# Performance work log

Measured on AMD Instinct MI355X. Metric: run time of the kernel, lower is better.

Reference implementation:

```python
import jax, jax.numpy as jnp
import numpy as np

B, S, D = 2, 512, 256      # batch, seq_len, d_model
N = 16                     # d_state
DC = 4                     # d_conv
DI = 2 * D                 # d_inner
CHUNK = 32                 # scan remat chunk size (S % CHUNK == 0)


def setup_inputs() -> dict:
    key = jax.random.key(0)
    ks = jax.random.split(key, 10)
    sc = 0.02
    return {
        "x": jax.random.normal(ks[0], (B, S, D), jnp.float32),
        "adjacency_matrix": jax.random.uniform(ks[1], (B, S, S), dtype=jnp.float32),
        "ln_w": jnp.ones((D,), jnp.float32),
        "ln_b": jnp.zeros((D,), jnp.float32),
        "W_in": jax.random.normal(ks[2], (2 * DI, D), jnp.float32) * sc,
        "conv_w": jax.random.normal(ks[3], (DI, DI, DC), jnp.float32) * sc,
        "conv_b": jnp.zeros((DI,), jnp.float32),
        "W_xp": jax.random.normal(ks[4], (2 * N + 1, DI), jnp.float32) * sc,
        "W_dt": jax.random.normal(ks[5], (DI, 1), jnp.float32) * sc,
        "b_dt": jnp.zeros((DI,), jnp.float32),
        "Wr": jax.random.normal(ks[6], (N, N), jnp.float32) * sc,
        "br": jnp.zeros((N,), jnp.float32),
        "W_out": jax.random.normal(ks[7], (D, DI), jnp.float32) * sc,
    }


def _forward(x, adj, ln_w, ln_b, W_in, conv_w, conv_b, W_xp, W_dt, b_dt, Wr, br, W_out):
    residual = x
    # LayerNorm (biased variance, eps=1e-5, matching nn.LayerNorm)
    mu = x.mean(-1, keepdims=True)
    var = ((x - mu) ** 2).mean(-1, keepdims=True)
    xn = (x - mu) * jax.lax.rsqrt(var + 1e-5) * ln_w + ln_b
    # in_proj (no bias), chunk into x branch and gate z
    xz = xn @ W_in.T                                  # [B,S,2*DI]
    xp, z = xz[..., :DI], xz[..., DI:]
    # causal-ish conv1d with padding d_conv-1, then slice to seq_len
    xc = jax.lax.conv_general_dilated(
        xp.transpose(0, 2, 1), conv_w, (1,), [(DC - 1, DC - 1)],
        dimension_numbers=("NCH", "OIH", "NCH"))
    xc = (xc + conv_b[None, :, None])[..., :S].transpose(0, 2, 1)  # [B,S,DI]
    x_act = jax.nn.silu(xc)
    # x_proj (no bias) -> delta(1), B(N), C(N)
    ssm = x_act @ W_xp.T                              # [B,S,2N+1]
    delta = jax.nn.softplus(ssm[..., :1] @ W_dt.T + b_dt)  # [B,S,DI]
    Bm, Cm = ssm[..., 1:1 + N], ssm[..., 1 + N:]      # [B,S,N]
    pos = jnp.arange(S)

    def step(carry, xs):
        h, hist = xs_carry = carry
        t, d_t, B_t, C_t, x_t, a_t = xs
        # exponential-decay state update: h [B,DI,N]
        h = h * jnp.exp(-d_t)[..., None] + x_t[..., None] * B_t[:, None, :]
        # adjacency-gated, degree-normalized aggregation over prior states
        w = a_t * (pos < t)                           # [B,S], zeros for s>=t
        deg = jnp.maximum(w.sum(-1), 1.0)             # clamp(min=1.0)
        g = jnp.einsum('bs,sbdn->bdn', w, hist) / deg[:, None, None]
        boost = 0.1 * jax.nn.silu(g @ Wr.T + br)
        # torch skips the boost when t==0 or all causal weights are zero
        h = h + jnp.where((t > 0) & jnp.any(w > 0), boost, jnp.zeros_like(boost))
        hist = hist.at[t].set(h)
        y = jnp.einsum('bdn,bn->bd', h, C_t)
        return (h, hist), y

    xs = (pos,
          delta.transpose(1, 0, 2), Bm.transpose(1, 0, 2), Cm.transpose(1, 0, 2),
          x_act.transpose(1, 0, 2), adj.transpose(1, 0, 2))
    nchunks = S // CHUNK
    xs = jax.tree_util.tree_map(lambda a: a.reshape(nchunks, CHUNK, *a.shape[1:]), xs)
    carry0 = (jnp.zeros((B, DI, N), jnp.float32),
              jnp.zeros((S, B, DI, N), jnp.float32))

    @jax.checkpoint
    def chunk_body(carry, xs_c):
        return jax.lax.scan(step, carry, xs_c)

    _, ys = jax.lax.scan(chunk_body, carry0, xs)
    y = ys.reshape(S, B, DI).transpose(1, 0, 2)       # [B,S,DI]
    return (y * jax.nn.silu(z)) @ W_out.T + residual


def reference(x, adjacency_matrix, ln_w, ln_b, W_in, conv_w, conv_b, W_xp, W_dt, b_dt, Wr, br, W_out):
    return _forward(x, adjacency_matrix, ln_w, ln_b, W_in, conv_w, conv_b,
                    W_xp, W_dt, b_dt, Wr, br, W_out)
```

## Files before the change

### kernel.cpp

```cpp
#include <hip/hip_runtime.h>
#include <math.h>

static constexpr int B  = 2;
static constexpr int S  = 512;
static constexpr int D  = 256;
static constexpr int N  = 16;
static constexpr int DI = 512;
static constexpr int CHUNK = 32;
static constexpr int NCHUNK = S / CHUNK;
static constexpr int NL = NCHUNK / 2;
static constexpr int DN = DI * N;
static constexpr int NSLOT = 8;

typedef unsigned int uint32;
typedef unsigned short ushort16;
using bf16x8 = __attribute__((ext_vector_type(8))) short;
using f32x4  = __attribute__((ext_vector_type(4))) float;

__device__ __forceinline__ ushort16 f2bf(float f) {
    uint32 u = __float_as_uint(f);
    u = (u + 0x7fffu + ((u >> 16) & 1u)) >> 16;
    return (ushort16)u;
}
__device__ __forceinline__ float bflo(uint32 u) { return __uint_as_float(u << 16); }
__device__ __forceinline__ float bfhi(uint32 u) { return __uint_as_float(u & 0xffff0000u); }
__device__ __forceinline__ float bf2f(ushort16 u) { return __uint_as_float(((uint32)u) << 16); }
__device__ __forceinline__ uint32 pk2(float a, float b) {
    return (uint32)(ushort16)f2bf(a) | ((uint32)(ushort16)f2bf(b) << 16);
}
template<int K>
__device__ __forceinline__ float rork(float x) {
    return __uint_as_float((uint32)__builtin_amdgcn_mov_dpp(
        (int)__float_as_uint(x), 0x120 + K, 0xf, 0xf, false));
}
__device__ __forceinline__ size_t htIdx(int b, int dn, int sb) {
    return ((size_t)(b * (S / 32) + sb) * DN + dn) * 32;
}

__global__ void ln_k(const float* __restrict__ x, const float* __restrict__ w,
                     const float* __restrict__ bias, ushort16* __restrict__ xnb) {
    int row = blockIdx.x;
    int lane = threadIdx.x;
    float4 v = *(const float4*)(x + row * D + lane * 4);
    float s = v.x + v.y + v.z + v.w;
    float q = v.x * v.x + v.y * v.y + v.z * v.z + v.w * v.w;
    for (int m = 1; m < 64; m <<= 1) { s += __shfl_xor(s, m); q += __shfl_xor(q, m); }
    float mu  = s * (1.0f / D);
    float var = q * (1.0f / D) - mu * mu;
    float rs  = rsqrtf(var + 1e-5f);
    float4 wv = *(const float4*)(w + lane * 4);
    float4 bv = *(const float4*)(bias + lane * 4);
    float4 o;
    o.x = (v.x - mu) * rs * wv.x + bv.x;
    o.y = (v.y - mu) * rs * wv.y + bv.y;
    o.z = (v.z - mu) * rs * wv.z + bv.z;
    o.w = (v.w - mu) * rs * wv.w + bv.w;
    uint2 pk;
    pk.x = pk2(o.x, o.y);
    pk.y = pk2(o.z, o.w);
    *(uint2*)(xnb + row * D + lane * 4) = pk;
}

template<int MODE>
__global__ __launch_bounds__(256) void gemmb_k(const ushort16* __restrict__ A,
                                               const float* __restrict__ W,
                                               const float* __restrict__ res,
                                               float* __restrict__ C,
                                               ushort16* __restrict__ xpb,
                                               float* __restrict__ zs,
                                               int M, int Nc, int K) {
    __shared__ __align__(16) short As[64 * 40];
    __shared__ __align__(16) short Ws[64 * 40];
    int tid = threadIdx.x;
    int l = tid & 63, wid = tid >> 6;
    int wm = wid & 1, wn = wid >> 1;
    int row0 = blockIdx.y * 64, col0 = blockIdx.x * 64;
    int r = tid >> 2, kseg = (tid & 3) * 8;
    f32x4 acc[2][2] = {};
    for (int k0 = 0; k0 < K; k0 += 32) {
        *(uint4*)&As[r * 40 + kseg] = *(const uint4*)(A + (size_t)(row0 + r) * K + k0 + kseg);
        {
            const float* wrow = W + (size_t)(col0 + r) * K + k0 + kseg;
            float4 w0 = *(const float4*)wrow;
            float4 w1 = *(const float4*)(wrow + 4);
            uint4 q;
            q.x = pk2(w0.x, w0.y); q.y = pk2(w0.z, w0.w);
            q.z = pk2(w1.x, w1.y); q.w = pk2(w1.z, w1.w);
            *(uint4*)&Ws[r * 40 + kseg] = q;
        }
        __syncthreads();
        bf16x8 aF[2], bF[2];
        #pragma unroll
        for (int am = 0; am < 2; ++am)
            aF[am] = *(const bf16x8*)&As[(wm * 32 + am * 16 + (l & 15)) * 40 + (l >> 4) * 8];
        #pragma unroll
        for (int bn = 0; bn < 2; ++bn)
            bF[bn] = *(const bf16x8*)&Ws[(wn * 32 + bn * 16 + (l & 15)) * 40 + (l >> 4) * 8];
        #pragma unroll
        for (int am = 0; am < 2; ++am)
            #pragma unroll
            for (int bn = 0; bn < 2; ++bn)
                acc[am][bn] = __builtin_amdgcn_mfma_f32_16x16x32_bf16(aF[am], bF[bn], acc[am][bn], 0, 0, 0);
        __syncthreads();
    }
    #pragma unroll
    for (int am = 0; am < 2; ++am)
        #pragma unroll
        for (int bn = 0; bn < 2; ++bn) {
            int cc = col0 + wn * 32 + bn * 16 + (l & 15);
            #pragma unroll
            for (int reg = 0; reg < 4; ++reg) {
                int rr = row0 + wm * 32 + am * 16 + (l >> 4) * 4 + reg;
                float v = acc[am][bn][reg];
                if (MODE == 0) {
                    if (res) v += res[(size_t)rr * Nc + cc];
                    C[(size_t)rr * Nc + cc] = v;
                } else {
                    int b = rr >> 9, t = rr & (S - 1);
                    if (cc < DI)
                        xpb[((size_t)(b * (S + 3) + 3 + t)) * DI + cc] = f2bf(v);
                    else
                        zs[((size_t)(b * S + t)) * DI + (cc - DI)] = v / (1.0f + __expf(-v));
                }
            }
        }
}

__global__ __launch_bounds__(256) void convm_k(const ushort16* __restrict__ xpb,
                                               const float* __restrict__ conv_w,
                                               const float* __restrict__ conv_b,
                                               float* __restrict__ x_act) {
    __shared__ __align__(16) short AxS[35 * 40];
    __shared__ __align__(16) short WbS[4 * 32 * 40];
    int tid = threadIdx.x;
    int l = tid & 63, wid = tid >> 6;
    int wm = wid & 1, wn = wid >> 1;
    int o0 = blockIdx.x * 32;
    int mt = blockIdx.y;
    int b = mt >> 4, tl0 = (mt & 15) * 32;
    f32x4 acc = {0.f, 0.f, 0.f, 0.f};

    for (int k0 = 0; k0 < DI; k0 += 32) {
        if (tid < 140) {
            int rr = tid >> 2, seg = tid & 3;
            uint4 v = *(const uint4*)(xpb + ((size_t)(b * (S + 3) + tl0 + rr)) * DI + k0 + seg * 8);
            *(uint4*)&AxS[rr * 40 + seg * 8] = v;
        }
        #pragma unroll
        for (int it = 0; it < 4; ++it) {
            int p = it * 256 + tid;
            int o = p >> 5, i = p & 31;
            float4 w4 = *(const float4*)(conv_w + ((size_t)(o0 + o) * DI + (k0 + i)) * 4);
            WbS[(0 * 32 + o) * 40 + i] = (short)f2bf(w4.x);
            WbS[(1 * 32 + o) * 40 + i] = (short)f2bf(w4.y);
            WbS[(2 * 32 + o) * 40 + i] = (short)f2bf(w4.z);
            WbS[(3 * 32 + o) * 40 + i] = (short)f2bf(w4.w);
        }
        __syncthreads();
        #pragma unroll
        for (int k = 0; k < 4; ++k) {
            bf16x8 aF = *(const bf16x8*)&AxS[(wm * 16 + (l & 15) + k) * 40 + (l >> 4) * 8];
            bf16x8 bF = *(const bf16x8*)&WbS[(k * 32 + wn * 16 + (l & 15)) * 40 + (l >> 4) * 8];
            acc = __builtin_amdgcn_mfma_f32_16x16x32_bf16(aF, bF, acc, 0, 0, 0);
        }
        __syncthreads();
    }
    int oc = o0 + wn * 16 + (l & 15);
    float bia = conv_b[oc];
    #pragma unroll
    for (int reg = 0; reg < 4; ++reg) {
        int m = wm * 16 + (l >> 4) * 4 + reg;
        float v = acc[reg] + bia;
        x_act[((size_t)(b * S + tl0 + m)) * DI + oc] = v / (1.0f + __expf(-v));
    }
}

__global__ void ssmE_k(const float* __restrict__ x_act, const float* __restrict__ W_xp,
                       const float* __restrict__ W_dt, const float* __restrict__ b_dt,
                       float* __restrict__ Bm, float* __restrict__ Cm,
                       float* __restrict__ E) {
    int row = blockIdx.x * 4 + (threadIdx.x >> 6);
    int lane = threadIdx.x & 63;
    const float* xr = x_act + (size_t)row * DI + lane * 8;
    float4 v0 = *(const float4*)xr;
    float4 v1 = *(const float4*)(xr + 4);
    float dtr = 0.0f;
    for (int j = 0; j < 2 * N + 1; ++j) {
        const float* wr = W_xp + (size_t)j * DI + lane * 8;
        float4 w0 = *(const float4*)wr;
        float4 w1 = *(const float4*)(wr + 4);
        float acc = v0.x * w0.x + v0.y * w0.y + v0.z * w0.z + v0.w * w0.w
                  + v1.x * w1.x + v1.y * w1.y + v1.z * w1.z + v1.w * w1.w;
        for (int m = 1; m < 64; m <<= 1) acc += __shfl_xor(acc, m);
        if (j == 0) dtr = acc;
        if (lane == 0) {
            if (j >= 1 && j < 1 + N) Bm[(size_t)row * N + (j - 1)] = acc;
            else if (j >= 1 + N)     Cm[(size_t)row * N + (j - 1 - N)] = acc;
        }
    }
    int d0 = lane * 8;
    float4 w0 = *(const float4*)(W_dt + d0);
    float4 w1 = *(const float4*)(W_dt + d0 + 4);
    float4 q0 = *(const float4*)(b_dt + d0);
    float4 q1 = *(const float4*)(b_dt + d0 + 4);
    float4 e0, e1;
    e0.x = 1.0f / (1.0f + __expf(dtr * w0.x + q0.x));
    e0.y = 1.0f / (1.0f + __expf(dtr * w0.y + q0.y));
    e0.z = 1.0f / (1.0f + __expf(dtr * w0.z + q0.z));
    e0.w = 1.0f / (1.0f + __expf(dtr * w0.w + q0.w));
    e1.x = 1.0f / (1.0f + __expf(dtr * w1.x + q1.x));
    e1.y = 1.0f / (1.0f + __expf(dtr * w1.y + q1.y));
    e1.z = 1.0f / (1.0f + __expf(dtr * w1.z + q1.z));
    e1.w = 1.0f / (1.0f + __expf(dtr * w1.w + q1.w));
    *(float4*)(E + (size_t)row * DI + d0) = e0;
    *(float4*)(E + (size_t)row * DI + d0 + 4) = e1;
}

__global__ void deg_k(const float* __restrict__ adj, float* __restrict__ rdeg, int* __restrict__ flagI) {
    int t = blockIdx.x & (S - 1), b = blockIdx.x >> 9;
    int lane = threadIdx.x;
    const float* row = adj + ((size_t)(b * S + t)) * S;
    float s = 0.0f; bool anyp = false;
    for (int i = lane; i < t; i += 64) { float v = row[i]; s += v; anyp |= (v > 0.0f); }
    for (int m = 1; m < 64; m <<= 1) s += __shfl_xor(s, m);
    bool any = __any(anyp);
    if (lane == 0) {
        rdeg[b * S + t] = 1.0f / fmaxf(s, 1.0f);
        if (t > 0 && any) atomicOr(flagI + t, 1);
    }
}

#define SCAN32(RO, ADJT, GSUM)                                              \
    _Pragma("unroll")                                                       \
    for (int j = 0; j < CHUNK; ++j) {                                       \
        float e  = eL [((RO) + j) * 8 + grp];                               \
        float xa = xaL[((RO) + j) * 8 + grp];                               \
        float Bn = BnL[((RO) + j) * 16 + n];                                \
        h = h * e + xa * Bn;                                                \
        float g0 = GSUM[j], g1 = 0.f, g2 = 0.f, g3 = 0.f;                   \
        const float* ar = (ADJT) + j * 36;                                  \
        int sp = 0;                                                         \
        _Pragma("unroll")                                                   \
        for (; sp + 4 <= j; sp += 4) {                                      \
            float4 av = *(const float4*)(ar + sp);                          \
            g0 += av.x * hreg[sp];     g1 += av.y * hreg[sp + 1];           \
            g2 += av.z * hreg[sp + 2]; g3 += av.w * hreg[sp + 3];           \
        }                                                                   \
        _Pragma("unroll")                                                   \
        for (; sp < j; ++sp) g0 += ar[sp] * hreg[sp];                       \
        float gr = (g0 + g1) + (g2 + g3);                                   \
        float m0 = gr * wrr[0] + rork<4>(gr) * wrr[4]                       \
                 + rork<8>(gr) * wrr[8] + rork<12>(gr) * wrr[12];           \
        float m1 = rork<1>(gr) * wrr[1] + rork<5>(gr) * wrr[5]              \
                 + rork<9>(gr) * wrr[9] + rork<13>(gr) * wrr[13];           \
        float m2 = rork<2>(gr) * wrr[2] + rork<6>(gr) * wrr[6]              \
                 + rork<10>(gr) * wrr[10] + rork<14>(gr) * wrr[14];         \
        float m3 = rork<3>(gr) * wrr[3] + rork<7>(gr) * wrr[7]              \
                 + rork<11>(gr) * wrr[11] + rork<15>(gr) * wrr[15];         \
        float acc = fmaf(rdegL[(RO) + j], (m0 + m1) + (m2 + m3), brn);      \
        if (flL[(RO) + j])                                                  \
            h = fmaf(0.1f * acc,                                            \
                     __builtin_amdgcn_rcpf(1.0f + __expf(-acc)), h);        \
        hreg[j] = h;                                                        \
    }

#define PRESUM(GSUM, PTR) {                                                 \
    const ushort16* _p = (PTR);                                             \
    _Pragma("unroll")                                                       \
    for (int qi = 0; qi < 4; ++qi) {                                        \
        uint4 q = *(const uint4*)(_p + qi * 8);                             \
        GSUM[qi*8+0] += bflo(q.x); GSUM[qi*8+1] += bfhi(q.x);               \
        GSUM[qi*8+2] += bflo(q.y); GSUM[qi*8+3] += bfhi(q.y);               \
        GSUM[qi*8+4] += bflo(q.z); GSUM[qi*8+5] += bfhi(q.z);               \
        GSUM[qi*8+6] += bflo(q.w); GSUM[qi*8+7] += bfhi(q.w);               \
    } }

__global__ __launch_bounds__(256) void chunk2_k(const float* __restrict__ adj,
                                                const float* __restrict__ x_act,
                                                const float* __restrict__ E,
                                                const float* __restrict__ Bm,
                                                const float* __restrict__ rdeg,
                                                const int* __restrict__ flagI,
                                                const float* __restrict__ Wr,
                                                const float* __restrict__ br,
                                                ushort16* __restrict__ Gall,
                                                ushort16* __restrict__ histT,
                                                float* __restrict__ hlast, int lc) {
    __shared__ __align__(16) char smem[56320];
    int tid = threadIdx.x;
    int cbA = 2 * lc * CHUNK;
    int cbB = cbA + CHUNK;
    const size_t SLOT = (size_t)B * DN * 32;
    int rp = lc & 1, wp = (lc + 1) & 1;

    if (blockIdx.x < 128) {
        float* adjA  = (float*)smem;
        float* adjB  = (float*)(smem + 4608);
        short* AsM   = (short*)(smem + 9216);
        short* AsT   = (short*)(smem + 11776);
        float* eL    = (float*)(smem + 22016);
        float* xaL   = (float*)(smem + 24064);
        float* BnL   = (float*)(smem + 26112);
        float* rdegL = (float*)(smem + 30208);
        int*   flL   = (int*)  (smem + 30464);
        short* hTA   = (short*)(smem + 31232);
        float* Gmid  = (float*)(smem + 39424);
        short* hTB   = (short*)(smem + 39424);

        int b = blockIdx.x >> 6;
        int d0 = (blockIdx.x & 63) << 3;
        int n = tid & 15, grp = tid >> 4;
        int d = d0 + (grp & 7);
        int dn = d * N + n;
        int dnbase = (blockIdx.x & 63) << 7;

        {
            int j = tid >> 3, s4 = (tid & 7) * 4;
            {
                float4 a0 = *(const float4*)(adj + ((size_t)(b * S + cbA + j)) * S + cbA + s4);
                float* dp = adjA + j * 36 + s4;
                dp[0] = a0.x; dp[1] = a0.y; dp[2] = a0.z; dp[3] = a0.w;
            }
            {
                float4 a0 = *(const float4*)(adj + ((size_t)(b * S + cbB + j)) * S + cbB + s4);
                float* dp = adjB + j * 36 + s4;
                dp[0] = a0.x; dp[1] = a0.y; dp[2] = a0.z; dp[3] = a0.w;
            }
            {
                float4 a0 = *(const float4*)(adj + ((size_t)(b * S + cbB + j)) * S + cbA + s4);
                uint2 q; q.x = pk2(a0.x, a0.y); q.y = pk2(a0.z, a0.w);
                *(uint2*)&AsM[j * 40 + s4] = q;
            }
            if (lc < NL - 1) {
                #pragma unroll
                for (int st = 0; st < 4; ++st) {
                    int src = st >> 1, tgt = st & 1;
                    float4 a0 = *(const float4*)(adj + ((size_t)(b * S + cbA + 64 + 32 * tgt + j)) * S
                                                 + cbA + 32 * src + s4);
                    uint2 q; q.x = pk2(a0.x, a0.y); q.y = pk2(a0.z, a0.w);
                    *(uint2*)&AsT[(src * 2 + tgt) * 1280 + j * 40 + s4] = q;
                }
            }
            int jr = tid >> 2, dd = (tid & 3) * 2;
            float2 ev = *(const float2*)(E     + ((size_t)(b * S + cbA + jr)) * DI + d0 + dd);
            float2 xv = *(const float2*)(x_act + ((size_t)(b * S + cbA + jr)) * DI + d0 + dd);
            eL [jr * 8 + dd] = ev.x; eL [jr * 8 + dd + 1] = ev.y;
            xaL[jr * 8 + dd] = xv.x; xaL[jr * 8 + dd + 1] = xv.y;
            int nn = (tid & 3) * 4;
            float4 bv = *(const float4*)(Bm + ((size_t)(b * S + cbA + jr)) * N + nn);
            BnL[jr * 16 + nn] = bv.x; BnL[jr * 16 + nn + 1] = bv.y;
            BnL[jr * 16 + nn + 2] = bv.z; BnL[jr * 16 + nn + 3] = bv.w;
            if (tid < 64) {
                rdegL[tid] = rdeg[b * S + cbA + tid];
                flL[tid]   = flagI[cbA + tid];
            }
        }
        __syncthreads();
        if (tid >= 128) return;

        float gsA[CHUNK], gsB[CHUNK];
        #pragma unroll
        for (int j = 0; j < CHUNK; ++j) { gsA[j] = 0.f; gsB[j] = 0.f; }
        {
            size_t tb = ((size_t)b * DN + dn) * 32;
            if (lc >= 2) {
                PRESUM(gsA, Gall + ((size_t)rp * NSLOT + 0) * SLOT + tb);
                PRESUM(gsA, Gall + ((size_t)rp * NSLOT + 1) * SLOT + tb);
                PRESUM(gsB, Gall + ((size_t)rp * NSLOT + 2) * SLOT + tb);
                PRESUM(gsB, Gall + ((size_t)rp * NSLOT + 3) * SLOT + tb);
            }
            if (lc >= 1) {
                PRESUM(gsA, Gall + ((size_t)rp * NSLOT + 4) * SLOT + tb);
                PRESUM(gsA, Gall + ((size_t)rp * NSLOT + 6) * SLOT + tb);
                PRESUM(gsB, Gall + ((size_t)rp * NSLOT + 5) * SLOT + tb);
                PRESUM(gsB, Gall + ((size_t)rp * NSLOT + 7) * SLOT + tb);
            }
        }

        int probe = __builtin_amdgcn_mov_dpp((int)n, 0x121, 0xf, 0xf, false);
        bool plusdir = (probe == ((n + 1) & 15));
        float wrr[16];
        #pragma unroll
        for (int k = 0; k < 16; ++k) {
            int ip = (n + k) & 15, im = (n - k + 16) & 15;
            wrr[k] = Wr[n * 16 + (plusdir ? ip : im)];
        }
        float brn = br[n];
        float h = (lc == 0) ? 0.0f : hlast[b * DN + dn];

        float hreg[CHUNK];
        SCAN32(0, adjA, gsA)

        {
            ushort16* ht = histT + htIdx(b, dn, 2 * lc);
            #pragma unroll
            for (int qi = 0; qi < 4; ++qi) {
                uint4 q;
                q.x = pk2(hreg[qi*8+0], hreg[qi*8+1]);
                q.y = pk2(hreg[qi*8+2], hreg[qi*8+3]);
                q.z = pk2(hreg[qi*8+4], hreg[qi*8+5]);
                q.w = pk2(hreg[qi*8+6], hreg[qi*8+7]);
                *(uint4*)(ht + qi * 8) = q;
                *(uint4*)&hTA[qi * 1024 + tid * 8] = q;
            }
        }
        __syncthreads();
        {
            int w = tid >> 6, l = tid & 63;
            bf16x8 aF0 = *(const bf16x8*)&AsM[(l & 15) * 40 + (l >> 4) * 8];
            bf16x8 aF1 = *(const bf16x8*)&AsM[(16 + (l & 15)) * 40 + (l >> 4) * 8];
            #pragma unroll
            for (int dblk = 0; dblk < 4; ++dblk) {
                int col = w * 64 + dblk * 16 + (l & 15);
                bf16x8 bF = *(const bf16x8*)&hTA[(l >> 4) * 1024 + col * 8];
                f32x4 a0v = {0.f,0.f,0.f,0.f}, a1v = {0.f,0.f,0.f,0.f};
                a0v = __builtin_amdgcn_mfma_f32_16x16x32_bf16(aF0, bF, a0v, 0, 0, 0);
                a1v = __builtin_amdgcn_mfma_f32_16x16x32_bf16(aF1, bF, a1v, 0, 0, 0);
                int jb0 = (l >> 4) * 4;
                #pragma unroll
                for (int reg = 0; reg < 4; ++reg) {
                    Gmid[(jb0 + reg) * 129 + col]      = a0v[reg];
                    Gmid[(16 + jb0 + reg) * 129 + col] = a1v[reg];
                }
            }
        }
        __syncthreads();
        #pragma unroll
        for (int j = 0; j < CHUNK; ++j) gsB[j] += Gmid[j * 129 + tid];
        __syncthreads();

        SCAN32(32, adjB, gsB)
        hlast[b * DN + dn] = h;

        {
            ushort16* ht = histT + htIdx(b, dn, 2 * lc + 1);
            #pragma unroll
            for (int qi = 0; qi < 4; ++qi) {
                uint4 q;
                q.x = pk2(hreg[qi*8+0], hreg[qi*8+1]);
                q.y = pk2(hreg[qi*8+2], hreg[qi*8+3]);
                q.z = pk2(hreg[qi*8+4], hreg[qi*8+5]);
                q.w = pk2(hreg[qi*8+6], hreg[qi*8+7]);
                *(uint4*)(ht + qi * 8) = q;
                *(uint4*)&hTB[qi * 1024 + tid * 8] = q;
            }
        }
        if (lc < NL - 1) {
            __syncthreads();
            int w = tid >> 6, l = tid & 63;
            int jb0 = (l >> 4) * 4;
            #pragma unroll
            for (int src = 0; src < 2; ++src) {
                const short* hTs = src ? hTB : hTA;
                #pragma unroll
                for (int tgt = 0; tgt < 2; ++tgt) {
                    const short* At = AsT + (src * 2 + tgt) * 1280;
                    bf16x8 aF0 = *(const bf16x8*)&At[(l & 15) * 40 + (l >> 4) * 8];
                    bf16x8 aF1 = *(const bf16x8*)&At[(16 + (l & 15)) * 40 + (l >> 4) * 8];
                    ushort16* gw = Gall + ((size_t)wp * NSLOT + (4 + src * 2 + tgt)) * SLOT;
                    #pragma unroll
                    for (int dblk = 0; dblk < 4; ++dblk) {
                        int col = w * 64 + dblk * 16 + (l & 15);
                        bf16x8 bF = *(const bf16x8*)&hTs[(l >> 4) * 1024 + col * 8];
                        f32x4 a0v = {0.f,0.f,0.f,0.f}, a1v = {0.f,0.f,0.f,0.f};
                        a0v = __builtin_amdgcn_mfma_f32_16x16x32_bf16(aF0, bF, a0v, 0, 0, 0);
                        a1v = __builtin_amdgcn_mfma_f32_16x16x32_bf16(aF1, bF, a1v, 0, 0, 0);
                        int dng = dnbase + col;
                        uint2 o0, o1;
                        o0.x = pk2(a0v[0], a0v[1]); o0.y = pk2(a0v[2], a0v[3]);
                        o1.x = pk2(a1v[0], a1v[1]); o1.y = pk2(a1v[2], a1v[3]);
                        *(uint2*)(gw + ((size_t)b * DN + dng) * 32 + jb0) = o0;
                        *(uint2*)(gw + ((size_t)b * DN + dng) * 32 + 16 + jb0) = o1;
                    }
                }
            }
        }
    } else {
        if (lc == 0 || lc >= NL - 1) return;
        int idx = blockIdx.x - 128;
        int tile = idx & 63;
        int b = (idx >> 6) & 1;
        int tgt = (idx >> 7) & 1;
        int kh = idx >> 8;
        int tc = 2 * lc + 2 + tgt;
        int ks0 = kh ? lc : 0;
        int ks1 = kh ? 2 * lc : lc;
        int dn0 = tile * 128;
        int w = tid >> 6, l = tid & 63;
        int jh = w & 1, dh = w >> 1;
        int kseg = (l >> 4) * 8;
        const float* abase = adj + ((size_t)(b * S + tc * CHUNK + jh * 16 + (l & 15))) * S + kseg;
        int dnrow = dn0 + dh * 64 + (l & 15);
        f32x4 acc[4] = {};
        #pragma unroll 2
        for (int ks = ks0; ks < ks1; ++ks) {
            float4 af0 = *(const float4*)(abase + ks * 32);
            float4 af1 = *(const float4*)(abase + ks * 32 + 4);
            uint4 aP;
            aP.x = pk2(af0.x, af0.y); aP.y = pk2(af0.z, af0.w);
            aP.z = pk2(af1.x, af1.y); aP.w = pk2(af1.z, af1.w);
            bf16x8 aF;
            *(uint4*)&aF = aP;
            uint4 bP[4];
            #pragma unroll
            for (int dblk = 0; dblk < 4; ++dblk)
                bP[dblk] = *(const uint4*)(histT + htIdx(b, dnrow + dblk * 16, ks) + kseg);
            #pragma unroll
            for (int dblk = 0; dblk < 4; ++dblk) {
                bf16x8 bF;
                *(uint4*)&bF = bP[dblk];
                acc[dblk] = __builtin_amdgcn_mfma_f32_16x16x32_bf16(aF, bF, acc[dblk], 0, 0, 0);
            }
        }
        int jb = jh * 16 + (l >> 4) * 4;
        ushort16* gbase = Gall + ((size_t)wp * NSLOT + (tgt * 2 + kh)) * SLOT;
        #pragma unroll
        for (int dblk = 0; dblk < 4; ++dblk) {
            int dnc = dn0 + dh * 64 + dblk * 16 + (l & 15);
            uint2 o;
            o.x = pk2(acc[dblk][0], acc[dblk][1]);
            o.y = pk2(acc[dblk][2], acc[dblk][3]);
            *(uint2*)(gbase + ((size_t)b * DN + dnc) * 32 + jb) = o;
        }
    }
}

__global__ __launch_bounds__(256) void y_k(const ushort16* __restrict__ histT,
                                           const float* __restrict__ Cm,
                                           const float* __restrict__ zs,
                                           ushort16* __restrict__ yzb) {
    __shared__ float CmL[S * 17];
    int b = blockIdx.x >> 9;
    int d = blockIdx.x & (DI - 1);
    int tid = threadIdx.x;
    #pragma unroll
    for (int q = 0; q < 8; ++q) {
        int l0 = q * 1024 + tid * 4;
        int t = l0 >> 4, n0 = l0 & 15;
        float4 v = *(const float4*)(Cm + (size_t)b * S * N + l0);
        CmL[t * 17 + n0]     = v.x;
        CmL[t * 17 + n0 + 1] = v.y;
        CmL[t * 17 + n0 + 2] = v.z;
        CmL[t * 17 + n0 + 3] = v.w;
    }
    __syncthreads();
    #pragma unroll
    for (int pass = 0; pass < 2; ++pass) {
        int t = pass * 256 + tid;
        int sb = t >> 5, si = t & 31;
        const ushort16* hb = histT + htIdx(b, d * N, sb) + si;
        float a0 = 0.f, a1 = 0.f, a2 = 0.f, a3 = 0.f;
        #pragma unroll
        for (int n = 0; n < 16; n += 4) {
            a0 += bf2f(hb[(size_t)n * 32])       * CmL[t * 17 + n];
            a1 += bf2f(hb[(size_t)(n + 1) * 32]) * CmL[t * 17 + n + 1];
            a2 += bf2f(hb[(size_t)(n + 2) * 32]) * CmL[t * 17 + n + 2];
            a3 += bf2f(hb[(size_t)(n + 3) * 32]) * CmL[t * 17 + n + 3];
        }
        float acc = (a0 + a1) + (a2 + a3);
        float zv = zs[((size_t)(b * S + t)) * DI + d];
        yzb[((size_t)(b * S + t)) * DI + d] = f2bf(acc * zv);
    }
}

extern "C" void kernel_launch(void* const* d_in, const int* in_sizes, int n_in,
                              void* d_out, int out_size, void* d_ws, size_t ws_size,
                              hipStream_t stream) {
    const float* x      = (const float*)d_in[0];
    const float* adj    = (const float*)d_in[1];
    const float* ln_w   = (const float*)d_in[2];
    const float* ln_b   = (const float*)d_in[3];
    const float* W_in   = (const float*)d_in[4];
    const float* conv_w = (const float*)d_in[5];
    const float* conv_b = (const float*)d_in[6];
    const float* W_xp   = (const float*)d_in[7];
    const float* W_dt   = (const float*)d_in[8];
    const float* b_dt   = (const float*)d_in[9];
    const float* Wr     = (const float*)d_in[10];
    const float* br     = (const float*)d_in[11];
    const float* W_out  = (const float*)d_in[12];
    float* out = (float*)d_out;

    float* ws = (float*)d_ws;
    size_t off = 0;
    float* x_act  = ws + off; off += (size_t)B * S * DI;
    float* Bmb    = ws + off; off += (size_t)B * S * N;
    float* Cmb    = ws + off; off += (size_t)B * S * N;
    float* rdegp  = ws + off; off += (size_t)B * S;
    int*   flagI  = (int*)(ws + off); off += S;
    float* Ebuf   = ws + off; off += (size_t)B * S * DI;
    float* zsbuf  = ws + off; off += (size_t)B * S * DI;
    float* hlast  = ws + off; off += (size_t)B * DN;
    ushort16* xnb    = (ushort16*)(ws + off); off += (size_t)B * S * D / 2;
    ushort16* yzb    = (ushort16*)(ws + off); off += (size_t)B * S * DI / 2;
    ushort16* histT  = (ushort16*)(ws + off); off += (size_t)B * DN * S / 2;
    ushort16* Gall   = (ushort16*)(ws + off); off += (size_t)2 * NSLOT * B * DN * 32 / 2;
    ushort16* xpb    = (ushort16*)(ws + off); off += (size_t)B * (S + 3) * DI / 2;

    hipMemsetAsync(flagI, 0, S * sizeof(int), stream);
    hipMemsetAsync(xpb, 0, (size_t)B * (S + 3) * DI * 2, stream);

    ln_k<<<B * S, 64, 0, stream>>>(x, ln_w, ln_b, xnb);
    gemmb_k<1><<<dim3(2 * DI / 64, B * S / 64), 256, 0, stream>>>(
        xnb, W_in, nullptr, nullptr, xpb, zsbuf, B * S, 2 * DI, D);
    convm_k<<<dim3(DI / 32, B * S / 32), 256, 0, stream>>>(xpb, conv_w, conv_b, x_act);
    ssmE_k<<<B * S / 4, 256, 0, stream>>>(x_act, W_xp, W_dt, b_dt, Bmb, Cmb, Ebuf);
    deg_k<<<B * S, 64, 0, stream>>>(adj, rdegp, flagI);

    for (int lc = 0; lc < NL; ++lc)
        chunk2_k<<<640, 256, 0, stream>>>(adj, x_act, Ebuf, Bmb, rdegp, flagI,
                                          Wr, br, Gall, histT, hlast, lc);

    y_k<<<B * DI, 256, 0, stream>>>(histT, Cmb, zsbuf, yzb);

    gemmb_k<0><<<dim3(D / 64, B * S / 64), 256, 0, stream>>>(
        yzb, W_out, x, out, nullptr, nullptr, B * S, D, DI);
}
```

Before: 265.5 us.

## Process four chunks per launch in the sequential scan kernel

The scan kernel now handles four 32-step chunks per launch instead of two, which halves the number of sequential launches (from 8 to 4). Intra-launch cross-chunk contributions are computed with MFMA against histories staged in shared memory, and more Gall slots (20) carry the next launch's contributions. The aim is to cut launch and serialization overhead on the critical path. In exchange there are more block-wide syncs per launch, more serial work inside each block, and fewer parallel helper blocks doing the long-range GEMM.

```diff
diff --git a/kernel.cpp b/kernel.cpp
--- a/kernel.cpp
+++ b/kernel.cpp
@@ -8,9 +8,9 @@
 static constexpr int DI = 512;
 static constexpr int CHUNK = 32;
 static constexpr int NCHUNK = S / CHUNK;
-static constexpr int NL = NCHUNK / 2;
+static constexpr int NL2 = 4;
 static constexpr int DN = DI * N;
-static constexpr int NSLOT = 8;
+static constexpr int NSLOT = 20;
 
 typedef unsigned int uint32;
 typedef unsigned short ushort16;
@@ -275,7 +275,63 @@
         GSUM[qi*8+6] += bflo(q.w); GSUM[qi*8+7] += bfhi(q.w);               \
     } }
 
-__global__ __launch_bounds__(256) void chunk2_k(const float* __restrict__ adj,
+#define HWRITE(CIDX, HTBUF) {                                               \
+    ushort16* ht = histT + htIdx(b, dn, (CIDX));                            \
+    _Pragma("unroll")                                                       \
+    for (int qi = 0; qi < 4; ++qi) {                                        \
+        uint4 q;                                                            \
+        q.x = pk2(hreg[qi*8+0], hreg[qi*8+1]);                              \
+        q.y = pk2(hreg[qi*8+2], hreg[qi*8+3]);                              \
+        q.z = pk2(hreg[qi*8+4], hreg[qi*8+5]);                              \
+        q.w = pk2(hreg[qi*8+6], hreg[qi*8+7]);                              \
+        *(uint4*)(ht + qi * 8) = q;                                         \
+        *(uint4*)&(HTBUF)[qi * 1024 + tid * 8] = q;                         \
+    } }
+
+#define MIDPHASE(TCL) {                                                     \
+    int w = tid >> 6, l = tid & 63;                                         \
+    int ksg = (l >> 4) * 8;                                                 \
+    f32x4 ac0[4] = {}, ac1[4] = {};                                         \
+    _Pragma("unroll")                                                       \
+    for (int sidx = 0; sidx < (TCL); ++sidx) {                              \
+        const float* p0 = adj + ((size_t)(b * S + c0s + (TCL) * 32 + (l & 15))) * S \
+                        + c0s + sidx * 32 + ksg;                            \
+        const float* p1 = p0 + 16 * S;                                      \
+        float4 a00 = *(const float4*)p0, a01 = *(const float4*)(p0 + 4);    \
+        float4 a10 = *(const float4*)p1, a11 = *(const float4*)(p1 + 4);    \
+        uint4 qa, qb;                                                       \
+        qa.x = pk2(a00.x, a00.y); qa.y = pk2(a00.z, a00.w);                 \
+        qa.z = pk2(a01.x, a01.y); qa.w = pk2(a01.z, a01.w);                 \
+        qb.x = pk2(a10.x, a10.y); qb.y = pk2(a10.z, a10.w);                 \
+        qb.z = pk2(a11.x, a11.y); qb.w = pk2(a11.z, a11.w);                 \
+        bf16x8 aF0, aF1;                                                    \
+        *(uint4*)&aF0 = qa; *(uint4*)&aF1 = qb;                             \
+        const short* hTs = hTarr[sidx];                                     \
+        _Pragma("unroll")                                                   \
+        for (int dblk = 0; dblk < 4; ++dblk) {                              \
+            int col = w * 64 + dblk * 16 + (l & 15);                        \
+            bf16x8 bF = *(const bf16x8*)&hTs[(l >> 4) * 1024 + col * 8];    \
+            ac0[dblk] = __builtin_amdgcn_mfma_f32_16x16x32_bf16(aF0, bF, ac0[dblk], 0, 0, 0); \
+            ac1[dblk] = __builtin_amdgcn_mfma_f32_16x16x32_bf16(aF1, bF, ac1[dblk], 0, 0, 0); \
+        }                                                                   \
+    }                                                                       \
+    int jb0 = (l >> 4) * 4;                                                 \
+    _Pragma("unroll")                                                       \
+    for (int dblk = 0; dblk < 4; ++dblk) {                                  \
+        int col = w * 64 + dblk * 16 + (l & 15);                            \
+        _Pragma("unroll")                                                   \
+        for (int reg = 0; reg < 4; ++reg) {                                 \
+            Gmid[(jb0 + reg) * 136 + col]      = (short)f2bf(ac0[dblk][reg]); \
+            Gmid[(16 + jb0 + reg) * 136 + col] = (short)f2bf(ac1[dblk][reg]); \
+        }                                                                   \
+    } }
+
+#define GSADD(GSUM)                                                         \
+    _Pragma("unroll")                                                       \
+    for (int j = 0; j < CHUNK; ++j)                                         \
+        GSUM[j] += bf2f((ushort16)Gmid[j * 136 + tid]);
+
+__global__ __launch_bounds__(256) void chunk4_k(const float* __restrict__ adj,
                                                 const float* __restrict__ x_act,
                                                 const float* __restrict__ E,
                                                 const float* __restrict__ Bm,
@@ -286,214 +342,225 @@
                                                 ushort16* __restrict__ Gall,
                                                 ushort16* __restrict__ histT,
                                                 float* __restrict__ hlast, int lc) {
-    __shared__ __align__(16) char smem[56320];
+    __shared__ __align__(16) char smem[51200];
     int tid = threadIdx.x;
-    int cbA = 2 * lc * CHUNK;
-    int cbB = cbA + CHUNK;
+    int c0 = 4 * lc;
+    int c0s = c0 * CHUNK;
     const size_t SLOT = (size_t)B * DN * 32;
     int rp = lc & 1, wp = (lc + 1) & 1;
 
     if (blockIdx.x < 128) {
-        float* adjA  = (float*)smem;
-        float* adjB  = (float*)(smem + 4608);
-        short* AsM   = (short*)(smem + 9216);
-        short* AsT   = (short*)(smem + 11776);
-        float* eL    = (float*)(smem + 22016);
-        float* xaL   = (float*)(smem + 24064);
-        float* BnL   = (float*)(smem + 26112);
-        float* rdegL = (float*)(smem + 30208);
-        int*   flL   = (int*)  (smem + 30464);
-        short* hTA   = (short*)(smem + 31232);
-        float* Gmid  = (float*)(smem + 39424);
-        short* hTB   = (short*)(smem + 39424);
+        float* triA  = (float*)smem;
+        float* triB  = (float*)(smem + 4608);
+        float* eL    = (float*)(smem + 9216);
+        float* xaL   = (float*)(smem + 11264);
+        float* BnL   = (float*)(smem + 13312);
+        float* rdegL = (float*)(smem + 17408);
+        int*   flL   = (int*)  (smem + 17664);
+        short* hTA   = (short*)(smem + 17920);
+        short* hTB   = (short*)(smem + 26112);
+        short* hTC   = (short*)(smem + 34304);
+        short* Gmid  = (short*)(smem + 42496);
+        short* hTD   = (short*)(smem + 42496);
 
         int b = blockIdx.x >> 6;
         int d0 = (blockIdx.x & 63) << 3;
-        int n = tid & 15, grp = tid >> 4;
-        int d = d0 + (grp & 7);
+        int n = tid & 15, grp = (tid >> 4) & 7;
+        int d = d0 + grp;
         int dn = d * N + n;
         int dnbase = (blockIdx.x & 63) << 7;
+        const short* hTarr[4] = {hTA, hTB, hTC, hTD};
 
         {
             int j = tid >> 3, s4 = (tid & 7) * 4;
             {
-                float4 a0 = *(const float4*)(adj + ((size_t)(b * S + cbA + j)) * S + cbA + s4);
-                float* dp = adjA + j * 36 + s4;
+                float4 a0 = *(const float4*)(adj + ((size_t)(b * S + c0s + j)) * S + c0s + s4);
+                float* dp = triA + j * 36 + s4;
                 dp[0] = a0.x; dp[1] = a0.y; dp[2] = a0.z; dp[3] = a0.w;
             }
             {
-                float4 a0 = *(const float4*)(adj + ((size_t)(b * S + cbB + j)) * S + cbB + s4);
-                float* dp = adjB + j * 36 + s4;
+                float4 a0 = *(const float4*)(adj + ((size_t)(b * S + c0s + 32 + j)) * S + c0s + 32 + s4);
+                float* dp = triB + j * 36 + s4;
                 dp[0] = a0.x; dp[1] = a0.y; dp[2] = a0.z; dp[3] = a0.w;
             }
-            {
-                float4 a0 = *(const float4*)(adj + ((size_t)(b * S + cbB + j)) * S + cbA + s4);
-                uint2 q; q.x = pk2(a0.x, a0.y); q.y = pk2(a0.z, a0.w);
-                *(uint2*)&AsM[j * 40 + s4] = q;
-            }
-            if (lc < NL - 1) {
-                #pragma unroll
-                for (int st = 0; st < 4; ++st) {
-                    int src = st >> 1, tgt = st & 1;
-                    float4 a0 = *(const float4*)(adj + ((size_t)(b * S + cbA + 64 + 32 * tgt + j)) * S
-                                                 + cbA + 32 * src + s4);
-                    uint2 q; q.x = pk2(a0.x, a0.y); q.y = pk2(a0.z, a0.w);
-                    *(uint2*)&AsT[(src * 2 + tgt) * 1280 + j * 40 + s4] = q;
-                }
-            }
             int jr = tid >> 2, dd = (tid & 3) * 2;
-            float2 ev = *(const float2*)(E     + ((size_t)(b * S + cbA + jr)) * DI + d0 + dd);
-            float2 xv = *(const float2*)(x_act + ((size_t)(b * S + cbA + jr)) * DI + d0 + dd);
+            float2 ev = *(const float2*)(E     + ((size_t)(b * S + c0s + jr)) * DI + d0 + dd);
+            float2 xv = *(const float2*)(x_act + ((size_t)(b * S + c0s + jr)) * DI + d0 + dd);
             eL [jr * 8 + dd] = ev.x; eL [jr * 8 + dd + 1] = ev.y;
             xaL[jr * 8 + dd] = xv.x; xaL[jr * 8 + dd + 1] = xv.y;
             int nn = (tid & 3) * 4;
-            float4 bv = *(const float4*)(Bm + ((size_t)(b * S + cbA + jr)) * N + nn);
+            float4 bv = *(const float4*)(Bm + ((size_t)(b * S + c0s + jr)) * N + nn);
             BnL[jr * 16 + nn] = bv.x; BnL[jr * 16 + nn + 1] = bv.y;
             BnL[jr * 16 + nn + 2] = bv.z; BnL[jr * 16 + nn + 3] = bv.w;
             if (tid < 64) {
-                rdegL[tid] = rdeg[b * S + cbA + tid];
-                flL[tid]   = flagI[cbA + tid];
-            }
-        }
-        __syncthreads();
-        if (tid >= 128) return;
-
-        float gsA[CHUNK], gsB[CHUNK];
-        #pragma unroll
-        for (int j = 0; j < CHUNK; ++j) { gsA[j] = 0.f; gsB[j] = 0.f; }
-        {
+                rdegL[tid] = rdeg[b * S + c0s + tid];
+                flL[tid]   = flagI[c0s + tid];
+            }
+        }
+        __syncthreads();
+
+        float gs0[CHUNK], gs1[CHUNK];
+        float wrr[16];
+        float brn = 0.f, h = 0.f;
+        float hreg[CHUNK];
+
+        if (tid < 128) {
+            #pragma unroll
+            for (int j = 0; j < CHUNK; ++j) { gs0[j] = 0.f; gs1[j] = 0.f; }
             size_t tb = ((size_t)b * DN + dn) * 32;
             if (lc >= 2) {
-                PRESUM(gsA, Gall + ((size_t)rp * NSLOT + 0) * SLOT + tb);
-                PRESUM(gsA, Gall + ((size_t)rp * NSLOT + 1) * SLOT + tb);
-                PRESUM(gsB, Gall + ((size_t)rp * NSLOT + 2) * SLOT + tb);
-                PRESUM(gsB, Gall + ((size_t)rp * NSLOT + 3) * SLOT + tb);
+                PRESUM(gs0, Gall + ((size_t)rp * NSLOT + 0) * SLOT + tb);
+                PRESUM(gs1, Gall + ((size_t)rp * NSLOT + 1) * SLOT + tb);
             }
             if (lc >= 1) {
-                PRESUM(gsA, Gall + ((size_t)rp * NSLOT + 4) * SLOT + tb);
-                PRESUM(gsA, Gall + ((size_t)rp * NSLOT + 6) * SLOT + tb);
-                PRESUM(gsB, Gall + ((size_t)rp * NSLOT + 5) * SLOT + tb);
-                PRESUM(gsB, Gall + ((size_t)rp * NSLOT + 7) * SLOT + tb);
-            }
-        }
-
-        int probe = __builtin_amdgcn_mov_dpp((int)n, 0x121, 0xf, 0xf, false);
-        bool plusdir = (probe == ((n + 1) & 15));
-        float wrr[16];
-        #pragma unroll
-        for (int k = 0; k < 16; ++k) {
-            int ip = (n + k) & 15, im = (n - k + 16) & 15;
-            wrr[k] = Wr[n * 16 + (plusdir ? ip : im)];
-        }
-        float brn = br[n];
-        float h = (lc == 0) ? 0.0f : hlast[b * DN + dn];
-
-        float hreg[CHUNK];
-        SCAN32(0, adjA, gsA)
+                #pragma unroll
+                for (int src = 0; src < 4; ++src) {
+                    PRESUM(gs0, Gall + ((size_t)rp * NSLOT + (4 + src * 4 + 0)) * SLOT + tb);
+                    PRESUM(gs1, Gall + ((size_t)rp * NSLOT + (4 + src * 4 + 1)) * SLOT + tb);
+                }
+            }
+            int probe = __builtin_amdgcn_mov_dpp((int)n, 0x121, 0xf, 0xf, false);
+            bool plusdir = (probe == ((n + 1) & 15));
+            #pragma unroll
+            for (int k = 0; k < 16; ++k) {
+                int ip = (n + k) & 15, im = (n - k + 16) & 15;
+                wrr[k] = Wr[n * 16 + (plusdir ? ip : im)];
+            }
+            brn = br[n];
+            h = (lc == 0) ? 0.0f : hlast[b * DN + dn];
+
+            SCAN32(0, triA, gs0)
+            HWRITE(c0 + 0, hTA)
+        }
+        __syncthreads();
+        if (tid < 128) MIDPHASE(1)
+        __syncthreads();
+        if (tid < 128) {
+            GSADD(gs1)
+            SCAN32(32, triB, gs1)
+            HWRITE(c0 + 1, hTB)
+        }
+        __syncthreads();
 
         {
-            ushort16* ht = histT + htIdx(b, dn, 2 * lc);
+            int j = tid >> 3, s4 = (tid & 7) * 4;
+            {
+                float4 a0 = *(const float4*)(adj + ((size_t)(b * S + c0s + 64 + j)) * S + c0s + 64 + s4);
+                float* dp = triA + j * 36 + s4;
+                dp[0] = a0.x; dp[1] = a0.y; dp[2] = a0.z; dp[3] = a0.w;
+            }
+            {
+                float4 a0 = *(const float4*)(adj + ((size_t)(b * S + c0s + 96 + j)) * S + c0s + 96 + s4);
+                float* dp = triB + j * 36 + s4;
+                dp[0] = a0.x; dp[1] = a0.y; dp[2] = a0.z; dp[3] = a0.w;
+            }
+            int jr = tid >> 2, dd = (tid & 3) * 2;
+            float2 ev = *(const float2*)(E     + ((size_t)(b * S + c0s + 64 + jr)) * DI + d0 + dd);
+            float2 xv = *(const float2*)(x_act + ((size_t)(b * S + c0s + 64 + jr)) * DI + d0 + dd);
+            eL [jr * 8 + dd] = ev.x; eL [jr * 8 + dd + 1] = ev.y;
+            xaL[jr * 8 + dd] = xv.x; xaL[jr * 8 + dd + 1] = xv.y;
+            int nn = (tid & 3) * 4;
+            float4 bv = *(const float4*)(Bm + ((size_t)(b * S + c0s + 64 + jr)) * N + nn);
+            BnL[jr * 16 + nn] = bv.x; BnL[jr * 16 + nn + 1] = bv.y;
+            BnL[jr * 16 + nn + 2] = bv.z; BnL[jr * 16 + nn + 3] = bv.w;
+            if (tid < 64) {
+                rdegL[tid] = rdeg[b * S + c0s + 64 + tid];
+                flL[tid]   = flagI[c0s + 64 + tid];
+            }
+        }
+        if (tid < 128) {
             #pragma unroll
-            for (int qi = 0; qi < 4; ++qi) {
-                uint4 q;
-                q.x = pk2(hreg[qi*8+0], hreg[qi*8+1]);
-                q.y = pk2(hreg[qi*8+2], hreg[qi*8+3]);
-                q.z = pk2(hreg[qi*8+4], hreg[qi*8+5]);
-                q.w = pk2(hreg[qi*8+6], hreg[qi*8+7]);
-                *(uint4*)(ht + qi * 8) = q;
-                *(uint4*)&hTA[qi * 1024 + tid * 8] = q;
-            }
-        }
-        __syncthreads();
-        {
-            int w = tid >> 6, l = tid & 63;
-            bf16x8 aF0 = *(const bf16x8*)&AsM[(l & 15) * 40 + (l >> 4) * 8];
-            bf16x8 aF1 = *(const bf16x8*)&AsM[(16 + (l & 15)) * 40 + (l >> 4) * 8];
-            #pragma unroll
-            for (int dblk = 0; dblk < 4; ++dblk) {
-                int col = w * 64 + dblk * 16 + (l & 15);
-                bf16x8 bF = *(const bf16x8*)&hTA[(l >> 4) * 1024 + col * 8];
-                f32x4 a0v = {0.f,0.f,0.f,0.f}, a1v = {0.f,0.f,0.f,0.f};
-                a0v = __builtin_amdgcn_mfma_f32_16x16x32_bf16(aF0, bF, a0v, 0, 0, 0);
-                a1v = __builtin_amdgcn_mfma_f32_16x16x32_bf16(aF1, bF, a1v, 0, 0, 0);
-                int jb0 = (l >> 4) * 4;
+            for (int j = 0; j < CHUNK; ++j) { gs0[j] = 0.f; gs1[j] = 0.f; }
+            size_t tb = ((size_t)b * DN + dn) * 32;
+            if (lc >= 2) {
+                PRESUM(gs0, Gall + ((size_t)rp * NSLOT + 2) * SLOT + tb);
+                PRESUM(gs1, Gall + ((size_t)rp * NSLOT + 3) * SLOT + tb);
+            }
+            if (lc >= 1) {
                 #pragma unroll
-                for (int reg = 0; reg < 4; ++reg) {
-                    Gmid[(jb0 + reg) * 129 + col]      = a0v[reg];
-                    Gmid[(16 + jb0 + reg) * 129 + col] = a1v[reg];
+                for (int src = 0; src < 4; ++src) {
+                    PRESUM(gs0, Gall + ((size_t)rp * NSLOT + (4 + src * 4 + 2)) * SLOT + tb);
+                    PRESUM(gs1, Gall + ((size_t)rp * NSLOT + (4 + src * 4 + 3)) * SLOT + tb);
                 }
             }
         }
         __syncthreads();
-        #pragma unroll
-        for (int j = 0; j < CHUNK; ++j) gsB[j] += Gmid[j * 129 + tid];
-        __syncthreads();
-
-        SCAN32(32, adjB, gsB)
-        hlast[b * DN + dn] = h;
-
-        {
-            ushort16* ht = histT + htIdx(b, dn, 2 * lc + 1);
-            #pragma unroll
-            for (int qi = 0; qi < 4; ++qi) {
-                uint4 q;
-                q.x = pk2(hreg[qi*8+0], hreg[qi*8+1]);
-                q.y = pk2(hreg[qi*8+2], hreg[qi*8+3]);
-                q.z = pk2(hreg[qi*8+4], hreg[qi*8+5]);
-                q.w = pk2(hreg[qi*8+6], hreg[qi*8+7]);
-                *(uint4*)(ht + qi * 8) = q;
-                *(uint4*)&hTB[qi * 1024 + tid * 8] = q;
-            }
-        }
-        if (lc < NL - 1) {
-            __syncthreads();
-            int w = tid >> 6, l = tid & 63;
+        if (tid < 128) MIDPHASE(2)
+        __syncthreads();
+        if (tid < 128) {
+            GSADD(gs0)
+            SCAN32(0, triA, gs0)
+            HWRITE(c0 + 2, hTC)
+        }
+        __syncthreads();
+        if (tid < 128) MIDPHASE(3)
+        __syncthreads();
+        if (tid < 128) GSADD(gs1)
+        __syncthreads();
+        if (tid < 128) {
+            SCAN32(32, triB, gs1)
+            HWRITE(c0 + 3, hTD)
+            hlast[b * DN + dn] = h;
+        }
+        __syncthreads();
+
+        if (lc < NL2 - 1) {
+            int half = tid >> 7;
+            int lt = tid & 127;
+            int w = lt >> 6, l = lt & 63;
+            int ksg = (l >> 4) * 8;
             int jb0 = (l >> 4) * 4;
-            #pragma unroll
-            for (int src = 0; src < 2; ++src) {
-                const short* hTs = src ? hTB : hTA;
+            #pragma unroll 2
+            for (int cc = 0; cc < 8; ++cc) {
+                int combo = half * 8 + cc;
+                int src = combo >> 2, tgt = combo & 3;
+                const short* hTs = hTarr[src];
+                const float* p0 = adj + ((size_t)(b * S + (4 * (lc + 1) + tgt) * 32 + (l & 15))) * S
+                                + (4 * lc + src) * 32 + ksg;
+                const float* p1 = p0 + 16 * S;
+                float4 a00 = *(const float4*)p0, a01 = *(const float4*)(p0 + 4);
+                float4 a10 = *(const float4*)p1, a11 = *(const float4*)(p1 + 4);
+                uint4 qa, qb;
+                qa.x = pk2(a00.x, a00.y); qa.y = pk2(a00.z, a00.w);
+                qa.z = pk2(a01.x, a01.y); qa.w = pk2(a01.z, a01.w);
+                qb.x = pk2(a10.x, a10.y); qb.y = pk2(a10.z, a10.w);
+                qb.z = pk2(a11.x, a11.y); qb.w = pk2(a11.z, a11.w);
+                bf16x8 aF0, aF1;
+                *(uint4*)&aF0 = qa; *(uint4*)&aF1 = qb;
+                ushort16* gw = Gall + ((size_t)wp * NSLOT + (4 + combo)) * SLOT;
                 #pragma unroll
-                for (int tgt = 0; tgt < 2; ++tgt) {
-                    const short* At = AsT + (src * 2 + tgt) * 1280;
-                    bf16x8 aF0 = *(const bf16x8*)&At[(l & 15) * 40 + (l >> 4) * 8];
-                    bf16x8 aF1 = *(const bf16x8*)&At[(16 + (l & 15)) * 40 + (l >> 4) * 8];
-                    ushort16* gw = Gall + ((size_t)wp * NSLOT + (4 + src * 2 + tgt)) * SLOT;
-                    #pragma unroll
-                    for (int dblk = 0; dblk < 4; ++dblk) {
-                        int col = w * 64 + dblk * 16 + (l & 15);
-                        bf16x8 bF = *(const bf16x8*)&hTs[(l >> 4) * 1024 + col * 8];
-                        f32x4 a0v = {0.f,0.f,0.f,0.f}, a1v = {0.f,0.f,0.f,0.f};
-                        a0v = __builtin_amdgcn_mfma_f32_16x16x32_bf16(aF0, bF, a0v, 0, 0, 0);
-                        a1v = __builtin_amdgcn_mfma_f32_16x16x32_bf16(aF1, bF, a1v, 0, 0, 0);
-                        int dng = dnbase + col;
-                        uint2 o0, o1;
-                        o0.x = pk2(a0v[0], a0v[1]); o0.y = pk2(a0v[2], a0v[3]);
-                        o1.x = pk2(a1v[0], a1v[1]); o1.y = pk2(a1v[2], a1v[3]);
-                        *(uint2*)(gw + ((size_t)b * DN + dng) * 32 + jb0) = o0;
-                        *(uint2*)(gw + ((size_t)b * DN + dng) * 32 + 16 + jb0) = o1;
-                    }
+                for (int dblk = 0; dblk < 4; ++dblk) {
+                    int col = w * 64 + dblk * 16 + (l & 15);
+                    bf16x8 bF = *(const bf16x8*)&hTs[(l >> 4) * 1024 + col * 8];
+                    f32x4 a0v = {0.f,0.f,0.f,0.f}, a1v = {0.f,0.f,0.f,0.f};
+                    a0v = __builtin_amdgcn_mfma_f32_16x16x32_bf16(aF0, bF, a0v, 0, 0, 0);
+                    a1v = __builtin_amdgcn_mfma_f32_16x16x32_bf16(aF1, bF, a1v, 0, 0, 0);
+                    int dng = dnbase + col;
+                    uint2 o0, o1;
+                    o0.x = pk2(a0v[0], a0v[1]); o0.y = pk2(a0v[2], a0v[3]);
+                    o1.x = pk2(a1v[0], a1v[1]); o1.y = pk2(a1v[2], a1v[3]);
+                    *(uint2*)(gw + ((size_t)b * DN + dng) * 32 + jb0) = o0;
+                    *(uint2*)(gw + ((size_t)b * DN + dng) * 32 + 16 + jb0) = o1;
                 }
             }
         }
     } else {
-        if (lc == 0 || lc >= NL - 1) return;
+        if (lc == 0 || lc >= NL2 - 1) return;
         int idx = blockIdx.x - 128;
         int tile = idx & 63;
         int b = (idx >> 6) & 1;
-        int tgt = (idx >> 7) & 1;
-        int kh = idx >> 8;
-        int tc = 2 * lc + 2 + tgt;
-        int ks0 = kh ? lc : 0;
-        int ks1 = kh ? 2 * lc : lc;
+        int tgt = idx >> 7;
+        int tc = 4 * (lc + 1) + tgt;
         int dn0 = tile * 128;
         int w = tid >> 6, l = tid & 63;
         int jh = w & 1, dh = w >> 1;
-        int kseg = (l >> 4) * 8;
-        const float* abase = adj + ((size_t)(b * S + tc * CHUNK + jh * 16 + (l & 15))) * S + kseg;
+        int ksg = (l >> 4) * 8;
+        const float* abase = adj + ((size_t)(b * S + tc * CHUNK + jh * 16 + (l & 15))) * S + ksg;
         int dnrow = dn0 + dh * 64 + (l & 15);
+        int K = 4 * lc;
         f32x4 acc[4] = {};
         #pragma unroll 2
-        for (int ks = ks0; ks < ks1; ++ks) {
+        for (int ks = 0; ks < K; ++ks) {
             float4 af0 = *(const float4*)(abase + ks * 32);
             float4 af1 = *(const float4*)(abase + ks * 32 + 4);
             uint4 aP;
@@ -504,7 +571,7 @@
             uint4 bP[4];
             #pragma unroll
             for (int dblk = 0; dblk < 4; ++dblk)
-                bP[dblk] = *(const uint4*)(histT + htIdx(b, dnrow + dblk * 16, ks) + kseg);
+                bP[dblk] = *(const uint4*)(histT + htIdx(b, dnrow + dblk * 16, ks) + ksg);
             #pragma unroll
             for (int dblk = 0; dblk < 4; ++dblk) {
                 bf16x8 bF;
@@ -513,7 +580,7 @@
             }
         }
         int jb = jh * 16 + (l >> 4) * 4;
-        ushort16* gbase = Gall + ((size_t)wp * NSLOT + (tgt * 2 + kh)) * SLOT;
+        ushort16* gbase = Gall + ((size_t)wp * NSLOT + tgt) * SLOT;
         #pragma unroll
         for (int dblk = 0; dblk < 4; ++dblk) {
             int dnc = dn0 + dh * 64 + dblk * 16 + (l & 15);
@@ -607,8 +674,8 @@
     ssmE_k<<<B * S / 4, 256, 0, stream>>>(x_act, W_xp, W_dt, b_dt, Bmb, Cmb, Ebuf);
     deg_k<<<B * S, 64, 0, stream>>>(adj, rdegp, flagI);
 
-    for (int lc = 0; lc < NL; ++lc)
-        chunk2_k<<<640, 256, 0, stream>>>(adj, x_act, Ebuf, Bmb, rdegp, flagI,
+    for (int lc = 0; lc < NL2; ++lc)
+        chunk4_k<<<640, 256, 0, stream>>>(adj, x_act, Ebuf, Bmb, rdegp, flagI,
                                           Wr, br, Gall, histT, hlast, lc);
 
     y_k<<<B * DI, 256, 0, stream>>>(histT, Cmb, zsbuf, yzb);
```

Measured after the change: 283.7 us. +6.9%, slower.
